# Performance work log

Measured on AMD Instinct MI355X. Metric: run time of the kernel, lower is better.

Reference implementation:

```python
import jax, jax.numpy as jnp
import numpy as np

B, N, H, E, M = 2, 20000, 256, 160000, 512


def setup_inputs() -> dict:
    key = jax.random.key(0)
    ks = jax.random.split(key, 8)
    s = 0.02  # small init scale like trained nets
    return {
        "h": jax.random.normal(ks[0], (B, N, H), jnp.float32),
        "edge_index": jax.random.randint(ks[1], (2, E), 0, N, jnp.int64),
        "msg_w1": jax.random.normal(ks[2], (2 * H, M), jnp.float32) * s,
        "msg_b1": jnp.zeros((M,), jnp.float32),
        "msg_w2": jax.random.normal(ks[3], (M, H), jnp.float32) * s,
        "msg_b2": jnp.zeros((H,), jnp.float32),
        "upd_w1": jax.random.normal(ks[4], (2 * H, M), jnp.float32) * s,
        "upd_b1": jnp.zeros((M,), jnp.float32),
        "upd_w2": jax.random.normal(ks[5], (M, H), jnp.float32) * s,
        "upd_b2": jnp.zeros((H,), jnp.float32),
    }


def _mlp(x, w1, b1, w2, b2):
    return jax.nn.relu(x @ w1 + b1) @ w2 + b2


def reference(h, edge_index, msg_w1, msg_b1, msg_w2, msg_b2,
              upd_w1, upd_b1, upd_w2, upd_b2):
    src, dst = edge_index[0], edge_index[1]
    h_src = h[:, src, :]                         # [B,E,H] gather
    h_dst = h[:, dst, :]                         # [B,E,H] gather
    m = _mlp(jnp.concatenate([h_src, h_dst], axis=-1),
             msg_w1, msg_b1, msg_w2, msg_b2)     # [B,E,H]
    agg = jnp.zeros_like(h).at[:, dst, :].add(m) # scatter-add over dst
    upd = _mlp(jnp.concatenate([h, agg], axis=-1),
               upd_w1, upd_b1, upd_w2, upd_b2)   # [B,N,H]
    return h + upd  # mp_residual=True
```

## Files before the change

kernel.cpp:

```cpp
#include <hip/hip_runtime.h>
#include <hip/hip_bf16.h>
#include <stdint.h>

#define B_ 2
#define N_ 20000
#define H_ 256
#define E_ 160000
#define M_ 512

typedef short bf16x8 __attribute__((ext_vector_type(8)));
typedef float f32x4 __attribute__((ext_vector_type(4)));

__device__ __forceinline__ unsigned short f2bf(float f) {
    union { float f; unsigned u; } cv; cv.f = f;
    unsigned u = cv.u;
    unsigned r = u + 0x7fffu + ((u >> 16) & 1u);
    return (unsigned short)(r >> 16);
}
__device__ __forceinline__ unsigned pack2(float a, float b) {
    return (unsigned)f2bf(a) | ((unsigned)f2bf(b) << 16);
}
__device__ __forceinline__ float bflo(unsigned p) {
    union { unsigned u; float f; } c; c.u = p << 16; return c.f;
}
__device__ __forceinline__ float bfhi(unsigned p) {
    union { unsigned u; float f; } c; c.u = p & 0xffff0000u; return c.f;
}

__device__ __forceinline__ void conv_t_one(const float* __restrict__ W,
                                           unsigned short* __restrict__ Wt,
                                           int K, int Ncol, int idx) {
    int n = idx % Ncol;
    int kc = (idx / Ncol) << 3;
    unsigned short t[8];
#pragma unroll
    for (int j = 0; j < 8; ++j) t[j] = f2bf(W[(size_t)(kc + j) * Ncol + n]);
    uint4 v;
    v.x = (unsigned)t[0] | ((unsigned)t[1] << 16);
    v.y = (unsigned)t[2] | ((unsigned)t[3] << 16);
    v.z = (unsigned)t[4] | ((unsigned)t[5] << 16);
    v.w = (unsigned)t[6] | ((unsigned)t[7] << 16);
    *(uint4*)(Wt + (size_t)n * K + kc) = v;
}

__device__ __forceinline__ void conv_w1pq_one(const float* __restrict__ W,
                                              unsigned short* __restrict__ Wt, int idx) {
    int jj = idx & 1023;
    int kc = (idx >> 10) << 3;
    int koff = (jj >= 512) ? 256 : 0;
    int j = jj & 511;
    unsigned short t[8];
#pragma unroll
    for (int r = 0; r < 8; ++r) t[r] = f2bf(W[(size_t)(kc + r + koff) * 512 + j]);
    uint4 v;
    v.x = (unsigned)t[0] | ((unsigned)t[1] << 16);
    v.y = (unsigned)t[2] | ((unsigned)t[3] << 16);
    v.z = (unsigned)t[4] | ((unsigned)t[5] << 16);
    v.w = (unsigned)t[6] | ((unsigned)t[7] << 16);
    *(uint4*)(Wt + (size_t)jj * 256 + kc) = v;
}

__global__ void conv_all(const float* __restrict__ mw1, const float* __restrict__ mw2,
                         const float* __restrict__ uw1, const float* __restrict__ uw2,
                         unsigned short* __restrict__ w1pq, unsigned short* __restrict__ w2t,
                         unsigned short* __restrict__ u1t, unsigned short* __restrict__ u2t) {
    int idx = blockIdx.x * blockDim.x + threadIdx.x;
    if (idx < 32768) {
        conv_w1pq_one(mw1, w1pq, idx);
    } else if (idx < 49152) {
        conv_t_one(mw2, w2t, 512, 256, idx - 32768);
    } else if (idx < 81920) {
        conv_t_one(uw1, u1t, 512, 512, idx - 49152);
    } else if (idx < 98304) {
        conv_t_one(uw2, u2t, 512, 256, idx - 81920);
    }
}

__global__ void hist_kernel(const int* __restrict__ eidx, int* __restrict__ cnt) {
    for (int e = blockIdx.x * blockDim.x + threadIdx.x; e < E_;
         e += gridDim.x * blockDim.x)
        atomicAdd(cnt + eidx[E_ + e], 1);
}

__global__ void scan_kernel(const int* __restrict__ cnt, int* __restrict__ offs,
                            int* __restrict__ cursor) {
    __shared__ int part[1024];
    int t = threadIdx.x;
    int base_i = t * 20;
    int loc[20];
    int s = 0;
#pragma unroll 20
    for (int i = 0; i < 20; ++i) {
        int idx = base_i + i;
        int v = (idx < N_) ? cnt[idx] : 0;
        loc[i] = s;
        s += v;
    }
    part[t] = s;
    __syncthreads();
    for (int off = 1; off < 1024; off <<= 1) {
        int tmp = (t >= off) ? part[t - off] : 0;
        __syncthreads();
        if (t >= off) part[t] += tmp;
        __syncthreads();
    }
    int base = part[t] - s;
#pragma unroll 20
    for (int i = 0; i < 20; ++i) {
        int idx = base_i + i;
        if (idx < N_) {
            int o = base + loc[i];
            offs[idx] = o;
            cursor[idx] = o;
        }
    }
    if (t == 1023) offs[N_] = part[1023];
}

__global__ void scatter_kernel(const int* __restrict__ eidx, int* __restrict__ cursor,
                               int* __restrict__ srcs) {
    for (int e = blockIdx.x * blockDim.x + threadIdx.x; e < E_;
         e += gridDim.x * blockDim.x) {
        int d = eidx[E_ + e];
        int pos = atomicAdd(cursor + d, 1);
        srcs[pos] = eidx[e];
    }
}

__global__ __launch_bounds__(512, 4) void pq_gemm(
    const float* __restrict__ hb,
    const unsigned short* __restrict__ W1pq,
    unsigned short* __restrict__ PQ) {
    __shared__ char smem[32 * 512];
    const int tid = threadIdx.x;
    const int tile = blockIdx.x >> 1;
    const int qh = blockIdx.x & 1;
    const int row0 = tile * 32;

#pragma unroll
    for (int it = 0; it < 4; ++it) {
        int linear = it * 512 + tid;
        int row = linear >> 6;
        int c4 = linear & 63;
        float4 v = *(const float4*)(hb + (size_t)(row0 + row) * H_ + c4 * 4);
        int byte = (row * 512 + c4 * 8) ^ ((row & 7) << 4);
        uint2 p;
        p.x = pack2(v.x, v.y);
        p.y = pack2(v.z, v.w);
        *(uint2*)(smem + byte) = p;
    }
    __syncthreads();

    const int lane = tid & 63;
    const int w = tid >> 6;
    const int lo = lane & 15;
    const int hi = lane >> 4;
    const int colw = qh * 512 + w * 64;

    f32x4 acc[2][4];
#pragma unroll
    for (int i = 0; i < 2; ++i)
#pragma unroll
        for (int j = 0; j < 4; ++j) acc[i][j] = (f32x4){0.f, 0.f, 0.f, 0.f};

#pragma unroll 4
    for (int ks = 0; ks < 256; ks += 32) {
        bf16x8 af[2];
#pragma unroll
        for (int rf = 0; rf < 2; ++rf) {
            int row = rf * 16 + lo;
            int byte = (row * 512 + (ks + 8 * hi) * 2) ^ ((row & 7) << 4);
            af[rf] = *(const bf16x8*)(smem + byte);
        }
#pragma unroll
        for (int cf = 0; cf < 4; ++cf) {
            bf16x8 bfr = *(const bf16x8*)(W1pq + (size_t)(colw + cf * 16 + lo) * 256 + ks + 8 * hi);
#pragma unroll
            for (int rf = 0; rf < 2; ++rf)
                acc[rf][cf] = __builtin_amdgcn_mfma_f32_16x16x32_bf16(af[rf], bfr, acc[rf][cf], 0, 0, 0);
        }
    }

#pragma unroll
    for (int cf = 0; cf < 4; ++cf) {
        int col = colw + cf * 16 + lo;
#pragma unroll
        for (int rf = 0; rf < 2; ++rf) {
#pragma unroll
            for (int r = 0; r < 4; ++r) {
                int row = rf * 16 + hi * 4 + r;
                PQ[(size_t)(row0 + row) * 1024 + col] = f2bf(acc[rf][cf][r]);
            }
        }
    }
}

__global__ __launch_bounds__(512, 4) void aggupd_kernel(
    const unsigned short* __restrict__ PQ,
    const int* __restrict__ srcs,
    const int* __restrict__ offs,
    const int* __restrict__ cnt,
    const unsigned short* __restrict__ w2t,
    const float* __restrict__ mb1,
    const float* __restrict__ mb2,
    const unsigned short* __restrict__ u1t,
    const float* __restrict__ ub1,
    const unsigned short* __restrict__ u2t,
    const float* __restrict__ ub2,
    const float* __restrict__ hb,
    float* __restrict__ outb) {
    __shared__ char smA[32 * 1024];
    __shared__ char smB[32 * 1024];
    __shared__ int s_cnt[32];

    const int tid = threadIdx.x;
    const int d0 = blockIdx.x * 32;

    if (tid < 32) s_cnt[tid] = cnt[d0 + tid];

#pragma unroll
    for (int it = 0; it < 2; ++it) {
        int linear = it * 512 + tid;
        int row = linear >> 5;
        int c8 = linear & 31;
        const float* src = hb + (size_t)(d0 + row) * H_ + c8 * 8;
        float4 a = *(const float4*)src;
        float4 b = *(const float4*)(src + 4);
        uint4 v;
        v.x = pack2(a.x, a.y);
        v.y = pack2(a.z, a.w);
        v.z = pack2(b.x, b.y);
        v.w = pack2(b.z, b.w);
        int byte = (row * 1024 + c8 * 16) ^ ((row & 7) << 4);
        *(uint4*)(smB + byte) = v;
    }

    const int dsub = tid >> 4;
    const int part = tid & 15;
    const int d = d0 + dsub;

    unsigned qb[16];
    {
        const unsigned short* qrow = PQ + (size_t)d * 1024 + 512;
#pragma unroll
        for (int c = 0; c < 4; ++c) {
            int cb = (c * 16 + part) * 8;
            bf16x8 qv = *(const bf16x8*)(qrow + cb);
#pragma unroll
            for (int jp = 0; jp < 4; ++jp) {
                float q0 = bflo((unsigned)(unsigned short)qv[jp * 2]) + mb1[cb + jp * 2];
                float q1 = bflo((unsigned)(unsigned short)qv[jp * 2 + 1]) + mb1[cb + jp * 2 + 1];
                qb[c * 4 + jp] = pack2(q0, q1);
            }
        }
    }

    float acc[32];
#pragma unroll
    for (int i = 0; i < 32; ++i) acc[i] = 0.f;

    const int beg = offs[d];
    const int end = offs[d + 1];
    int p = beg;
    for (; p + 1 < end; p += 2) {
        int s0 = srcs[p];
        int s1 = srcs[p + 1];
        const unsigned short* r0 = PQ + (size_t)s0 * 1024;
        const unsigned short* r1 = PQ + (size_t)s1 * 1024;
        bf16x8 v0[4], v1[4];
#pragma unroll
        for (int c = 0; c < 4; ++c) {
            v0[c] = *(const bf16x8*)(r0 + (c * 16 + part) * 8);
            v1[c] = *(const bf16x8*)(r1 + (c * 16 + part) * 8);
        }
#pragma unroll
        for (int c = 0; c < 4; ++c) {
#pragma unroll
            for (int jp = 0; jp < 4; ++jp) {
                unsigned q = qb[c * 4 + jp];
                float ql = bflo(q), qh2 = bfhi(q);
                acc[c * 8 + jp * 2] += fmaxf(bflo((unsigned)(unsigned short)v0[c][jp * 2]) + ql, 0.f)
                                     + fmaxf(bflo((unsigned)(unsigned short)v1[c][jp * 2]) + ql, 0.f);
                acc[c * 8 + jp * 2 + 1] += fmaxf(bflo((unsigned)(unsigned short)v0[c][jp * 2 + 1]) + qh2, 0.f)
                                         + fmaxf(bflo((unsigned)(unsigned short)v1[c][jp * 2 + 1]) + qh2, 0.f);
            }
        }
    }
    if (p < end) {
        int s0 = srcs[p];
        const unsigned short* r0 = PQ + (size_t)s0 * 1024;
#pragma unroll
        for (int c = 0; c < 4; ++c) {
            bf16x8 v0 = *(const bf16x8*)(r0 + (c * 16 + part) * 8);
#pragma unroll
            for (int jp = 0; jp < 4; ++jp) {
                unsigned q = qb[c * 4 + jp];
                acc[c * 8 + jp * 2]     += fmaxf(bflo((unsigned)(unsigned short)v0[jp * 2]) + bflo(q), 0.f);
                acc[c * 8 + jp * 2 + 1] += fmaxf(bflo((unsigned)(unsigned short)v0[jp * 2 + 1]) + bfhi(q), 0.f);
            }
        }
    }

#pragma unroll
    for (int c = 0; c < 4; ++c) {
        uint4 v;
        v.x = pack2(acc[c * 8 + 0], acc[c * 8 + 1]);
        v.y = pack2(acc[c * 8 + 2], acc[c * 8 + 3]);
        v.z = pack2(acc[c * 8 + 4], acc[c * 8 + 5]);
        v.w = pack2(acc[c * 8 + 6], acc[c * 8 + 7]);
        int byte = (dsub * 1024 + (c * 16 + part) * 16) ^ ((dsub & 7) << 4);
        *(uint4*)(smA + byte) = v;
    }
    __syncthreads();

    const int lane = tid & 63;
    const int w = tid >> 6;
    const int lo = lane & 15;
    const int hi = lane >> 4;

    {
        const int colw = w * 32;
        f32x4 a2[2][2];
#pragma unroll
        for (int i = 0; i < 2; ++i)
#pragma unroll
            for (int j = 0; j < 2; ++j) a2[i][j] = (f32x4){0.f, 0.f, 0.f, 0.f};

        for (int ks = 0; ks < 512; ks += 32) {
            bf16x8 af[2];
#pragma unroll
            for (int rf = 0; rf < 2; ++rf) {
                int row = rf * 16 + lo;
                int byte = (row * 1024 + (ks + 8 * hi) * 2) ^ ((row & 7) << 4);
                af[rf] = *(const bf16x8*)(smA + byte);
            }
#pragma unroll
            for (int cf = 0; cf < 2; ++cf) {
                bf16x8 bfr = *(const bf16x8*)(w2t + (size_t)(colw + cf * 16 + lo) * 512 + ks + 8 * hi);
#pragma unroll
                for (int rf = 0; rf < 2; ++rf)
                    a2[rf][cf] = __builtin_amdgcn_mfma_f32_16x16x32_bf16(af[rf], bfr, a2[rf][cf], 0, 0, 0);
            }
        }

#pragma unroll
        for (int cf = 0; cf < 2; ++cf) {
            int col = colw + cf * 16 + lo;
            float bb = mb2[col];
#pragma unroll
            for (int rf = 0; rf < 2; ++rf) {
#pragma unroll
                for (int r = 0; r < 4; ++r) {
                    int row = rf * 16 + hi * 4 + r;
                    float v = a2[rf][cf][r] + (float)s_cnt[row] * bb;
                    int byte = (row * 1024 + (256 + col) * 2) ^ ((row & 7) << 4);
                    *(unsigned short*)(smB + byte) = f2bf(v);
                }
            }
        }
    }
    __syncthreads();

    {
        const int colw = w * 64;
        f32x4 a1[2][4];
#pragma unroll
        for (int i = 0; i < 2; ++i)
#pragma unroll
            for (int j = 0; j < 4; ++j) a1[i][j] = (f32x4){0.f, 0.f, 0.f, 0.f};

        for (int ks = 0; ks < 512; ks += 32) {
            bf16x8 af[2];
#pragma unroll
            for (int rf = 0; rf < 2; ++rf) {
                int row = rf * 16 + lo;
                int byte = (row * 1024 + (ks + 8 * hi) * 2) ^ ((row & 7) << 4);
                af[rf] = *(const bf16x8*)(smB + byte);
            }
#pragma unroll
            for (int cf = 0; cf < 4; ++cf) {
                bf16x8 bfr = *(const bf16x8*)(u1t + (size_t)(colw + cf * 16 + lo) * 512 + ks + 8 * hi);
#pragma unroll
                for (int rf = 0; rf < 2; ++rf)
                    a1[rf][cf] = __builtin_amdgcn_mfma_f32_16x16x32_bf16(af[rf], bfr, a1[rf][cf], 0, 0, 0);
            }
        }

#pragma unroll
        for (int cf = 0; cf < 4; ++cf) {
            int col = colw + cf * 16 + lo;
            float bb = ub1[col];
#pragma unroll
            for (int rf = 0; rf < 2; ++rf) {
#pragma unroll
                for (int r = 0; r < 4; ++r) {
                    float v = fmaxf(a1[rf][cf][r] + bb, 0.f);
                    int row = rf * 16 + hi * 4 + r;
                    int byte = (row * 1024 + col * 2) ^ ((row & 7) << 4);
                    *(unsigned short*)(smA + byte) = f2bf(v);
                }
            }
        }
    }
    __syncthreads();

    {
        const int colw = w * 32;
        f32x4 a2[2][2];
#pragma unroll
        for (int i = 0; i < 2; ++i)
#pragma unroll
            for (int j = 0; j < 2; ++j) a2[i][j] = (f32x4){0.f, 0.f, 0.f, 0.f};

        for (int ks = 0; ks < 512; ks += 32) {
            bf16x8 af[2];
#pragma unroll
            for (int rf = 0; rf < 2; ++rf) {
                int row = rf * 16 + lo;
                int byte = (row * 1024 + (ks + 8 * hi) * 2) ^ ((row & 7) << 4);
                af[rf] = *(const bf16x8*)(smA + byte);
            }
#pragma unroll
            for (int cf = 0; cf < 2; ++cf) {
                bf16x8 bfr = *(const bf16x8*)(u2t + (size_t)(colw + cf * 16 + lo) * 512 + ks + 8 * hi);
#pragma unroll
                for (int rf = 0; rf < 2; ++rf)
                    a2[rf][cf] = __builtin_amdgcn_mfma_f32_16x16x32_bf16(af[rf], bfr, a2[rf][cf], 0, 0, 0);
            }
        }

#pragma unroll
        for (int cf = 0; cf < 2; ++cf) {
            int col = colw + cf * 16 + lo;
            float bb = ub2[col];
#pragma unroll
            for (int rf = 0; rf < 2; ++rf) {
#pragma unroll
                for (int r = 0; r < 4; ++r) {
                    int row = rf * 16 + hi * 4 + r;
                    size_t o = (size_t)(d0 + row) * H_ + col;
                    outb[o] = hb[o] + a2[rf][cf][r] + bb;
                }
            }
        }
    }
}

extern "C" void kernel_launch(void* const* d_in, const int* in_sizes, int n_in,
                              void* d_out, int out_size, void* d_ws, size_t ws_size,
                              hipStream_t stream) {
    const float* h      = (const float*)d_in[0];
    const int*   eidx   = (const int*)d_in[1];
    const float* msg_w1 = (const float*)d_in[2];
    const float* msg_b1 = (const float*)d_in[3];
    const float* msg_w2 = (const float*)d_in[4];
    const float* msg_b2 = (const float*)d_in[5];
    const float* upd_w1 = (const float*)d_in[6];
    const float* upd_b1 = (const float*)d_in[7];
    const float* upd_w2 = (const float*)d_in[8];
    const float* upd_b2 = (const float*)d_in[9];
    float* out = (float*)d_out;

    char* ws = (char*)d_ws;
    size_t off = 0;
    auto alloc = [&](size_t bytes) {
        char* p = ws + off;
        off = (off + bytes + 255) & ~(size_t)255;
        return p;
    };
    unsigned short* PQ   = (unsigned short*)alloc((size_t)N_ * 1024 * 2);
    unsigned short* w1pq = (unsigned short*)alloc(1024 * 256 * 2);
    unsigned short* w2t  = (unsigned short*)alloc(256 * 512 * 2);
    unsigned short* u1t  = (unsigned short*)alloc(512 * 512 * 2);
    unsigned short* u2t  = (unsigned short*)alloc(256 * 512 * 2);
    int* cnt    = (int*)alloc(N_ * 4);
    int* offs   = (int*)alloc((N_ + 1) * 4);
    int* cursor = (int*)alloc(N_ * 4);
    int* srcs   = (int*)alloc(E_ * 4);
    if (ws_size < off) return;

    hipMemsetAsync(cnt, 0, N_ * 4, stream);
    conv_all<<<384, 256, 0, stream>>>(msg_w1, msg_w2, upd_w1, upd_w2, w1pq, w2t, u1t, u2t);

    hist_kernel<<<256, 256, 0, stream>>>(eidx, cnt);
    scan_kernel<<<1, 1024, 0, stream>>>(cnt, offs, cursor);
    scatter_kernel<<<256, 256, 0, stream>>>(eidx, cursor, srcs);

    for (int b = 0; b < B_; ++b) {
        const float* hb = h + (size_t)b * N_ * H_;
        pq_gemm<<<(N_ / 32) * 2, 512, 0, stream>>>(hb, w1pq, PQ);
        aggupd_kernel<<<N_ / 32, 512, 0, stream>>>(PQ, srcs, offs, cnt, w2t,
                                                   msg_b1, msg_b2,
                                                   u1t, upd_b1, u2t, upd_b2,
                                                   hb, out + (size_t)b * N_ * H_);
    }
}
```

Measured before the change: 455.5 us.

## Double node tile to 64 rows in both GEMM kernels and reuse one LDS buffer

The node tile grows from 32 to 64 rows in pq_gemm and aggupd_kernel, so each weight fragment loaded from global memory feeds twice as many MFMAs, and bounds guards handle the ragged last tile. In the aggregation kernel, 8 threads per destination node now each keep 64 accumulators, and the Q half of PQ (plus the message bias) is staged in shared memory instead of registers. The second LDS buffer is removed by ordering the h load after the w2 GEMM into the same buffer. The cost is more registers and a single 64KB LDS buffer per block, which lowers occupancy and halves the number of blocks.

```diff
diff --git a/kernel.cpp b/kernel.cpp
--- a/kernel.cpp
+++ b/kernel.cpp
@@ -22,9 +22,6 @@
 }
 __device__ __forceinline__ float bflo(unsigned p) {
     union { unsigned u; float f; } c; c.u = p << 16; return c.f;
-}
-__device__ __forceinline__ float bfhi(unsigned p) {
-    union { unsigned u; float f; } c; c.u = p & 0xffff0000u; return c.f;
 }
 
 __device__ __forceinline__ void conv_t_one(const float* __restrict__ W,
@@ -131,18 +128,20 @@
     const float* __restrict__ hb,
     const unsigned short* __restrict__ W1pq,
     unsigned short* __restrict__ PQ) {
-    __shared__ char smem[32 * 512];
+    __shared__ char smem[64 * 512];
     const int tid = threadIdx.x;
     const int tile = blockIdx.x >> 1;
     const int qh = blockIdx.x & 1;
-    const int row0 = tile * 32;
-
-#pragma unroll
-    for (int it = 0; it < 4; ++it) {
+    const int row0 = tile * 64;
+
+#pragma unroll
+    for (int it = 0; it < 8; ++it) {
         int linear = it * 512 + tid;
         int row = linear >> 6;
         int c4 = linear & 63;
-        float4 v = *(const float4*)(hb + (size_t)(row0 + row) * H_ + c4 * 4);
+        int grow = row0 + row;
+        if (grow >= N_) grow = N_ - 1;
+        float4 v = *(const float4*)(hb + (size_t)grow * H_ + c4 * 4);
         int byte = (row * 512 + c4 * 8) ^ ((row & 7) << 4);
         uint2 p;
         p.x = pack2(v.x, v.y);
@@ -157,17 +156,17 @@
     const int hi = lane >> 4;
     const int colw = qh * 512 + w * 64;
 
-    f32x4 acc[2][4];
-#pragma unroll
-    for (int i = 0; i < 2; ++i)
+    f32x4 acc[4][4];
+#pragma unroll
+    for (int i = 0; i < 4; ++i)
 #pragma unroll
         for (int j = 0; j < 4; ++j) acc[i][j] = (f32x4){0.f, 0.f, 0.f, 0.f};
 
-#pragma unroll 4
+#pragma unroll
     for (int ks = 0; ks < 256; ks += 32) {
-        bf16x8 af[2];
-#pragma unroll
-        for (int rf = 0; rf < 2; ++rf) {
+        bf16x8 af[4];
+#pragma unroll
+        for (int rf = 0; rf < 4; ++rf) {
             int row = rf * 16 + lo;
             int byte = (row * 512 + (ks + 8 * hi) * 2) ^ ((row & 7) << 4);
             af[rf] = *(const bf16x8*)(smem + byte);
@@ -176,7 +175,7 @@
         for (int cf = 0; cf < 4; ++cf) {
             bf16x8 bfr = *(const bf16x8*)(W1pq + (size_t)(colw + cf * 16 + lo) * 256 + ks + 8 * hi);
 #pragma unroll
-            for (int rf = 0; rf < 2; ++rf)
+            for (int rf = 0; rf < 4; ++rf)
                 acc[rf][cf] = __builtin_amdgcn_mfma_f32_16x16x32_bf16(af[rf], bfr, acc[rf][cf], 0, 0, 0);
         }
     }
@@ -185,11 +184,12 @@
     for (int cf = 0; cf < 4; ++cf) {
         int col = colw + cf * 16 + lo;
 #pragma unroll
-        for (int rf = 0; rf < 2; ++rf) {
+        for (int rf = 0; rf < 4; ++rf) {
 #pragma unroll
             for (int r = 0; r < 4; ++r) {
                 int row = rf * 16 + hi * 4 + r;
-                PQ[(size_t)(row0 + row) * 1024 + col] = f2bf(acc[rf][cf][r]);
+                if (row0 + row < N_)
+                    PQ[(size_t)(row0 + row) * 1024 + col] = f2bf(acc[rf][cf][r]);
             }
         }
     }
@@ -209,21 +209,163 @@
     const float* __restrict__ ub2,
     const float* __restrict__ hb,
     float* __restrict__ outb) {
-    __shared__ char smA[32 * 1024];
-    __shared__ char smB[32 * 1024];
-    __shared__ int s_cnt[32];
+    __shared__ char smA[64 * 1024];
+    __shared__ int s_cnt[64];
 
     const int tid = threadIdx.x;
-    const int d0 = blockIdx.x * 32;
-
-    if (tid < 32) s_cnt[tid] = cnt[d0 + tid];
-
-#pragma unroll
-    for (int it = 0; it < 2; ++it) {
+    const int d0 = blockIdx.x * 64;
+
+    if (tid < 64) {
+        int dd = d0 + tid;
+        s_cnt[tid] = (dd < N_) ? cnt[dd] : 0;
+    }
+
+#pragma unroll
+    for (int it = 0; it < 8; ++it) {
+        int linear = it * 512 + tid;
+        int row = linear >> 6;
+        int c8 = linear & 63;
+        int dd = d0 + row;
+        if (dd >= N_) dd = N_ - 1;
+        bf16x8 qv = *(const bf16x8*)(PQ + (size_t)dd * 1024 + 512 + c8 * 8);
+        const float* bsrc = mb1 + c8 * 8;
+        uint4 v;
+        float q0, q1;
+        q0 = bflo((unsigned)(unsigned short)qv[0]) + bsrc[0];
+        q1 = bflo((unsigned)(unsigned short)qv[1]) + bsrc[1];
+        v.x = pack2(q0, q1);
+        q0 = bflo((unsigned)(unsigned short)qv[2]) + bsrc[2];
+        q1 = bflo((unsigned)(unsigned short)qv[3]) + bsrc[3];
+        v.y = pack2(q0, q1);
+        q0 = bflo((unsigned)(unsigned short)qv[4]) + bsrc[4];
+        q1 = bflo((unsigned)(unsigned short)qv[5]) + bsrc[5];
+        v.z = pack2(q0, q1);
+        q0 = bflo((unsigned)(unsigned short)qv[6]) + bsrc[6];
+        q1 = bflo((unsigned)(unsigned short)qv[7]) + bsrc[7];
+        v.w = pack2(q0, q1);
+        int byte = (row * 1024 + c8 * 16) ^ ((row & 7) << 4);
+        *(uint4*)(smA + byte) = v;
+    }
+    __syncthreads();
+
+    const int dsub = tid >> 3;
+    const int part = tid & 7;
+    {
+        const int d = d0 + dsub;
+        int beg = 0, end = 0;
+        if (d < N_) { beg = offs[d]; end = offs[d + 1]; }
+
+        float acc[64];
+#pragma unroll
+        for (int i = 0; i < 64; ++i) acc[i] = 0.f;
+
+        int p = beg;
+        for (; p + 1 < end; p += 2) {
+            int s0 = srcs[p];
+            int s1 = srcs[p + 1];
+            const unsigned short* r0 = PQ + (size_t)s0 * 1024;
+            const unsigned short* r1 = PQ + (size_t)s1 * 1024;
+#pragma unroll
+            for (int half = 0; half < 2; ++half) {
+                bf16x8 v0[4], v1[4];
+#pragma unroll
+                for (int c = 0; c < 4; ++c) {
+                    int ch = half * 4 + c;
+                    v0[c] = *(const bf16x8*)(r0 + (ch * 8 + part) * 8);
+                    v1[c] = *(const bf16x8*)(r1 + (ch * 8 + part) * 8);
+                }
+#pragma unroll
+                for (int c = 0; c < 4; ++c) {
+                    int ch = half * 4 + c;
+                    int byte = (dsub * 1024 + (ch * 8 + part) * 16) ^ ((dsub & 7) << 4);
+                    bf16x8 qv = *(const bf16x8*)(smA + byte);
+#pragma unroll
+                    for (int j = 0; j < 8; ++j) {
+                        float q = bflo((unsigned)(unsigned short)qv[j]);
+                        acc[ch * 8 + j] += fmaxf(bflo((unsigned)(unsigned short)v0[c][j]) + q, 0.f)
+                                         + fmaxf(bflo((unsigned)(unsigned short)v1[c][j]) + q, 0.f);
+                    }
+                }
+            }
+        }
+        if (p < end) {
+            int s0 = srcs[p];
+            const unsigned short* r0 = PQ + (size_t)s0 * 1024;
+#pragma unroll
+            for (int half = 0; half < 2; ++half) {
+                bf16x8 v0[4];
+#pragma unroll
+                for (int c = 0; c < 4; ++c) {
+                    int ch = half * 4 + c;
+                    v0[c] = *(const bf16x8*)(r0 + (ch * 8 + part) * 8);
+                }
+#pragma unroll
+                for (int c = 0; c < 4; ++c) {
+                    int ch = half * 4 + c;
+                    int byte = (dsub * 1024 + (ch * 8 + part) * 16) ^ ((dsub & 7) << 4);
+                    bf16x8 qv = *(const bf16x8*)(smA + byte);
+#pragma unroll
+                    for (int j = 0; j < 8; ++j) {
+                        float q = bflo((unsigned)(unsigned short)qv[j]);
+                        acc[ch * 8 + j] += fmaxf(bflo((unsigned)(unsigned short)v0[c][j]) + q, 0.f);
+                    }
+                }
+            }
+        }
+        __syncthreads();
+
+#pragma unroll
+        for (int c = 0; c < 8; ++c) {
+            uint4 v;
+            v.x = pack2(acc[c * 8 + 0], acc[c * 8 + 1]);
+            v.y = pack2(acc[c * 8 + 2], acc[c * 8 + 3]);
+            v.z = pack2(acc[c * 8 + 4], acc[c * 8 + 5]);
+            v.w = pack2(acc[c * 8 + 6], acc[c * 8 + 7]);
+            int byte = (dsub * 1024 + (c * 8 + part) * 16) ^ ((dsub & 7) << 4);
+            *(uint4*)(smA + byte) = v;
+        }
+    }
+    __syncthreads();
+
+    const int lane = tid & 63;
+    const int w = tid >> 6;
+    const int lo = lane & 15;
+    const int hi = lane >> 4;
+
+    f32x4 aB[4][2];
+#pragma unroll
+    for (int i = 0; i < 4; ++i)
+#pragma unroll
+        for (int j = 0; j < 2; ++j) aB[i][j] = (f32x4){0.f, 0.f, 0.f, 0.f};
+    {
+        const int colw = w * 32;
+        for (int ks = 0; ks < 512; ks += 32) {
+            bf16x8 af[4];
+#pragma unroll
+            for (int rf = 0; rf < 4; ++rf) {
+                int row = rf * 16 + lo;
+                int byte = (row * 1024 + (ks + 8 * hi) * 2) ^ ((row & 7) << 4);
+                af[rf] = *(const bf16x8*)(smA + byte);
+            }
+#pragma unroll
+            for (int cf = 0; cf < 2; ++cf) {
+                bf16x8 bfr = *(const bf16x8*)(w2t + (size_t)(colw + cf * 16 + lo) * 512 + ks + 8 * hi);
+#pragma unroll
+                for (int rf = 0; rf < 4; ++rf)
+                    aB[rf][cf] = __builtin_amdgcn_mfma_f32_16x16x32_bf16(af[rf], bfr, aB[rf][cf], 0, 0, 0);
+            }
+        }
+    }
+    __syncthreads();
+
+#pragma unroll
+    for (int it = 0; it < 4; ++it) {
         int linear = it * 512 + tid;
         int row = linear >> 5;
         int c8 = linear & 31;
-        const float* src = hb + (size_t)(d0 + row) * H_ + c8 * 8;
+        int grow = d0 + row;
+        if (grow >= N_) grow = N_ - 1;
+        const float* src = hb + (size_t)grow * H_ + c8 * 8;
         float4 a = *(const float4*)src;
         float4 b = *(const float4*)(src + 4);
         uint4 v;
@@ -232,130 +374,49 @@
         v.z = pack2(b.x, b.y);
         v.w = pack2(b.z, b.w);
         int byte = (row * 1024 + c8 * 16) ^ ((row & 7) << 4);
-        *(uint4*)(smB + byte) = v;
-    }
-
-    const int dsub = tid >> 4;
-    const int part = tid & 15;
-    const int d = d0 + dsub;
-
-    unsigned qb[16];
-    {
-        const unsigned short* qrow = PQ + (size_t)d * 1024 + 512;
-#pragma unroll
-        for (int c = 0; c < 4; ++c) {
-            int cb = (c * 16 + part) * 8;
-            bf16x8 qv = *(const bf16x8*)(qrow + cb);
-#pragma unroll
-            for (int jp = 0; jp < 4; ++jp) {
-                float q0 = bflo((unsigned)(unsigned short)qv[jp * 2]) + mb1[cb + jp * 2];
-                float q1 = bflo((unsigned)(unsigned short)qv[jp * 2 + 1]) + mb1[cb + jp * 2 + 1];
-                qb[c * 4 + jp] = pack2(q0, q1);
-            }
-        }
-    }
-
-    float acc[32];
-#pragma unroll
-    for (int i = 0; i < 32; ++i) acc[i] = 0.f;
-
-    const int beg = offs[d];
-    const int end = offs[d + 1];
-    int p = beg;
-    for (; p + 1 < end; p += 2) {
-        int s0 = srcs[p];
-        int s1 = srcs[p + 1];
-        const unsigned short* r0 = PQ + (size_t)s0 * 1024;
-        const unsigned short* r1 = PQ + (size_t)s1 * 1024;
-        bf16x8 v0[4], v1[4];
-#pragma unroll
-        for (int c = 0; c < 4; ++c) {
-            v0[c] = *(const bf16x8*)(r0 + (c * 16 + part) * 8);
-            v1[c] = *(const bf16x8*)(r1 + (c * 16 + part) * 8);
-        }
-#pragma unroll
-        for (int c = 0; c < 4; ++c) {
-#pragma unroll
-            for (int jp = 0; jp < 4; ++jp) {
-                unsigned q = qb[c * 4 + jp];
-                float ql = bflo(q), qh2 = bfhi(q);
-                acc[c * 8 + jp * 2] += fmaxf(bflo((unsigned)(unsigned short)v0[c][jp * 2]) + ql, 0.f)
-                                     + fmaxf(bflo((unsigned)(unsigned short)v1[c][jp * 2]) + ql, 0.f);
-                acc[c * 8 + jp * 2 + 1] += fmaxf(bflo((unsigned)(unsigned short)v0[c][jp * 2 + 1]) + qh2, 0.f)
-                                         + fmaxf(bflo((unsigned)(unsigned short)v1[c][jp * 2 + 1]) + qh2, 0.f);
-            }
-        }
-    }
-    if (p < end) {
-        int s0 = srcs[p];
-        const unsigned short* r0 = PQ + (size_t)s0 * 1024;
-#pragma unroll
-        for (int c = 0; c < 4; ++c) {
-            bf16x8 v0 = *(const bf16x8*)(r0 + (c * 16 + part) * 8);
-#pragma unroll
-            for (int jp = 0; jp < 4; ++jp) {
-                unsigned q = qb[c * 4 + jp];
-                acc[c * 8 + jp * 2]     += fmaxf(bflo((unsigned)(unsigned short)v0[jp * 2]) + bflo(q), 0.f);
-                acc[c * 8 + jp * 2 + 1] += fmaxf(bflo((unsigned)(unsigned short)v0[jp * 2 + 1]) + bfhi(q), 0.f);
-            }
-        }
-    }
-
-#pragma unroll
-    for (int c = 0; c < 4; ++c) {
-        uint4 v;
-        v.x = pack2(acc[c * 8 + 0], acc[c * 8 + 1]);
-        v.y = pack2(acc[c * 8 + 2], acc[c * 8 + 3]);
-        v.z = pack2(acc[c * 8 + 4], acc[c * 8 + 5]);
-        v.w = pack2(acc[c * 8 + 6], acc[c * 8 + 7]);
-        int byte = (dsub * 1024 + (c * 16 + part) * 16) ^ ((dsub & 7) << 4);
         *(uint4*)(smA + byte) = v;
     }
-    __syncthreads();
-
-    const int lane = tid & 63;
-    const int w = tid >> 6;
-    const int lo = lane & 15;
-    const int hi = lane >> 4;
-
     {
         const int colw = w * 32;
-        f32x4 a2[2][2];
-#pragma unroll
-        for (int i = 0; i < 2; ++i)
-#pragma unroll
-            for (int j = 0; j < 2; ++j) a2[i][j] = (f32x4){0.f, 0.f, 0.f, 0.f};
-
+#pragma unroll
+        for (int cf = 0; cf < 2; ++cf) {
+            int col = colw + cf * 16 + lo;
+            float bb = mb2[col];
+#pragma unroll
+            for (int rf = 0; rf < 4; ++rf) {
+#pragma unroll
+                for (int r = 0; r < 4; ++r) {
+                    int row = rf * 16 + hi * 4 + r;
+                    float v = aB[rf][cf][r] + (float)s_cnt[row] * bb;
+                    int byte = (row * 1024 + (256 + col) * 2) ^ ((row & 7) << 4);
+                    *(unsigned short*)(smA + byte) = f2bf(v);
+                }
+            }
+        }
+    }
+    __syncthreads();
+
+    f32x4 aC[4][4];
+#pragma unroll
+    for (int i = 0; i < 4; ++i)
+#pragma unroll
+        for (int j = 0; j < 4; ++j) aC[i][j] = (f32x4){0.f, 0.f, 0.f, 0.f};
+    {
+        const int colw = w * 64;
         for (int ks = 0; ks < 512; ks += 32) {
-            bf16x8 af[2];
-#pragma unroll
-            for (int rf = 0; rf < 2; ++rf) {
+            bf16x8 af[4];
+#pragma unroll
+            for (int rf = 0; rf < 4; ++rf) {
                 int row = rf * 16 + lo;
                 int byte = (row * 1024 + (ks + 8 * hi) * 2) ^ ((row & 7) << 4);
                 af[rf] = *(const bf16x8*)(smA + byte);
             }
 #pragma unroll
-            for (int cf = 0; cf < 2; ++cf) {
-                bf16x8 bfr = *(const bf16x8*)(w2t + (size_t)(colw + cf * 16 + lo) * 512 + ks + 8 * hi);
-#pragma unroll
-                for (int rf = 0; rf < 2; ++rf)
-                    a2[rf][cf] = __builtin_amdgcn_mfma_f32_16x16x32_bf16(af[rf], bfr, a2[rf][cf], 0, 0, 0);
-            }
-        }
-
-#pragma unroll
-        for (int cf = 0; cf < 2; ++cf) {
-            int col = colw + cf * 16 + lo;
-            float bb = mb2[col];
-#pragma unroll
-            for (int rf = 0; rf < 2; ++rf) {
-#pragma unroll
-                for (int r = 0; r < 4; ++r) {
-                    int row = rf * 16 + hi * 4 + r;
-                    float v = a2[rf][cf][r] + (float)s_cnt[row] * bb;
-                    int byte = (row * 1024 + (256 + col) * 2) ^ ((row & 7) << 4);
-                    *(unsigned short*)(smB + byte) = f2bf(v);
-                }
+            for (int cf = 0; cf < 4; ++cf) {
+                bf16x8 bfr = *(const bf16x8*)(u1t + (size_t)(colw + cf * 16 + lo) * 512 + ks + 8 * hi);
+#pragma unroll
+                for (int rf = 0; rf < 4; ++rf)
+                    aC[rf][cf] = __builtin_amdgcn_mfma_f32_16x16x32_bf16(af[rf], bfr, aC[rf][cf], 0, 0, 0);
             }
         }
     }
@@ -363,38 +424,15 @@
 
     {
         const int colw = w * 64;
-        f32x4 a1[2][4];
-#pragma unroll
-        for (int i = 0; i < 2; ++i)
-#pragma unroll
-            for (int j = 0; j < 4; ++j) a1[i][j] = (f32x4){0.f, 0.f, 0.f, 0.f};
-
-        for (int ks = 0; ks < 512; ks += 32) {
-            bf16x8 af[2];
-#pragma unroll
-            for (int rf = 0; rf < 2; ++rf) {
-                int row = rf * 16 + lo;
-                int byte = (row * 1024 + (ks + 8 * hi) * 2) ^ ((row & 7) << 4);
-                af[rf] = *(const bf16x8*)(smB + byte);
-            }
-#pragma unroll
-            for (int cf = 0; cf < 4; ++cf) {
-                bf16x8 bfr = *(const bf16x8*)(u1t + (size_t)(colw + cf * 16 + lo) * 512 + ks + 8 * hi);
-#pragma unroll
-                for (int rf = 0; rf < 2; ++rf)
-                    a1[rf][cf] = __builtin_amdgcn_mfma_f32_16x16x32_bf16(af[rf], bfr, a1[rf][cf], 0, 0, 0);
-            }
-        }
-
 #pragma unroll
         for (int cf = 0; cf < 4; ++cf) {
             int col = colw + cf * 16 + lo;
             float bb = ub1[col];
 #pragma unroll
-            for (int rf = 0; rf < 2; ++rf) {
+            for (int rf = 0; rf < 4; ++rf) {
 #pragma unroll
                 for (int r = 0; r < 4; ++r) {
-                    float v = fmaxf(a1[rf][cf][r] + bb, 0.f);
+                    float v = fmaxf(aC[rf][cf][r] + bb, 0.f);
                     int row = rf * 16 + hi * 4 + r;
                     int byte = (row * 1024 + col * 2) ^ ((row & 7) << 4);
                     *(unsigned short*)(smA + byte) = f2bf(v);
@@ -406,16 +444,16 @@
 
     {
         const int colw = w * 32;
-        f32x4 a2[2][2];
-#pragma unroll
-        for (int i = 0; i < 2; ++i)
-#pragma unroll
-            for (int j = 0; j < 2; ++j) a2[i][j] = (f32x4){0.f, 0.f, 0.f, 0.f};
+        f32x4 aD[4][2];
+#pragma unroll
+        for (int i = 0; i < 4; ++i)
+#pragma unroll
+            for (int j = 0; j < 2; ++j) aD[i][j] = (f32x4){0.f, 0.f, 0.f, 0.f};
 
         for (int ks = 0; ks < 512; ks += 32) {
-            bf16x8 af[2];
-#pragma unroll
-            for (int rf = 0; rf < 2; ++rf) {
+            bf16x8 af[4];
+#pragma unroll
+            for (int rf = 0; rf < 4; ++rf) {
                 int row = rf * 16 + lo;
                 int byte = (row * 1024 + (ks + 8 * hi) * 2) ^ ((row & 7) << 4);
                 af[rf] = *(const bf16x8*)(smA + byte);
@@ -424,8 +462,8 @@
             for (int cf = 0; cf < 2; ++cf) {
                 bf16x8 bfr = *(const bf16x8*)(u2t + (size_t)(colw + cf * 16 + lo) * 512 + ks + 8 * hi);
 #pragma unroll
-                for (int rf = 0; rf < 2; ++rf)
-                    a2[rf][cf] = __builtin_amdgcn_mfma_f32_16x16x32_bf16(af[rf], bfr, a2[rf][cf], 0, 0, 0);
+                for (int rf = 0; rf < 4; ++rf)
+                    aD[rf][cf] = __builtin_amdgcn_mfma_f32_16x16x32_bf16(af[rf], bfr, aD[rf][cf], 0, 0, 0);
             }
         }
 
@@ -434,12 +472,15 @@
             int col = colw + cf * 16 + lo;
             float bb = ub2[col];
 #pragma unroll
-            for (int rf = 0; rf < 2; ++rf) {
+            for (int rf = 0; rf < 4; ++rf) {
 #pragma unroll
                 for (int r = 0; r < 4; ++r) {
                     int row = rf * 16 + hi * 4 + r;
-                    size_t o = (size_t)(d0 + row) * H_ + col;
-                    outb[o] = hb[o] + a2[rf][cf][r] + bb;
+                    int grow = d0 + row;
+                    if (grow < N_) {
+                        size_t o = (size_t)grow * H_ + col;
+                        outb[o] = hb[o] + aD[rf][cf][r] + bb;
+                    }
                 }
             }
         }
@@ -486,12 +527,13 @@
     scan_kernel<<<1, 1024, 0, stream>>>(cnt, offs, cursor);
     scatter_kernel<<<256, 256, 0, stream>>>(eidx, cursor, srcs);
 
+    const int nblk = (N_ + 63) / 64;
     for (int b = 0; b < B_; ++b) {
         const float* hb = h + (size_t)b * N_ * H_;
-        pq_gemm<<<(N_ / 32) * 2, 512, 0, stream>>>(hb, w1pq, PQ);
-        aggupd_kernel<<<N_ / 32, 512, 0, stream>>>(PQ, srcs, offs, cnt, w2t,
-                                                   msg_b1, msg_b2,
-                                                   u1t, upd_b1, u2t, upd_b2,
-                                                   hb, out + (size_t)b * N_ * H_);
-    }
-}
+        pq_gemm<<<nblk * 2, 512, 0, stream>>>(hb, w1pq, PQ);
+        aggupd_kernel<<<nblk, 512, 0, stream>>>(PQ, srcs, offs, cnt, w2t,
+                                                msg_b1, msg_b2,
+                                                u1t, upd_b1, u2t, upd_b2,
+                                                hb, out + (size_t)b * N_ * H_);
+    }
+}
```

Result: slower. 502.4 us (+10.3%).
